# Performance work log

Hardware: AMD Instinct MI355X
Metric: run time of the kernel (lower is better)

The kernel has to match this reference:

```python
import jax, jax.numpy as jnp
import numpy as np

B, N, F, U = 4, 4096, 256, 128
NEG = -1.0e9


def setup_inputs() -> dict:
    key = jax.random.key(0)
    k1, k2, k3, k4, k5 = jax.random.split(key, 5)
    inputs = jax.random.normal(k1, (B, N, F), dtype=jnp.float32)
    # Glorot-normal-like scales
    w = jax.random.normal(k2, (F, U), dtype=jnp.float32) * np.sqrt(2.0 / (F + U)).astype(np.float32)
    ai = jax.random.normal(k3, (U, N), dtype=jnp.float32) * np.sqrt(2.0 / (U + N)).astype(np.float32)
    aj = jax.random.normal(k4, (U, N), dtype=jnp.float32) * np.sqrt(2.0 / (U + N)).astype(np.float32)
    a = (jax.random.uniform(k5, (N, N)) < 0.004).astype(jnp.float32)
    adj = jnp.maximum(a, a.T)
    return {"inputs": inputs, "w": w, "ai": ai, "aj": aj, "adj": adj}


def reference(inputs, w, ai, aj, adj):
    # f: [B, N, U]
    f = jnp.einsum('bnf,fu->bnu', inputs, w)
    # self_attn[b,i,j] = (f ai)[b,i,j]; other_attn = transpose([0,2,1]) of (f aj)
    self_attn = jnp.einsum('bnu,um->bnm', f, ai)          # [B, N, N]
    other_attn = jnp.einsum('bnu,um->bmn', f, aj)         # transposed [B, N, N]
    mask = adj + jnp.eye(N, dtype=adj.dtype)              # allow self + neighbors
    attn = self_attn + other_attn + NEG * (1.0 - mask)
    attn = jax.nn.softmax(attn, axis=1)                   # softmax over rows (axis=1)
    # out[b,j,u] = sum_i f[b,i,u] * attn[b,i,j]
    out = jnp.einsum('biu,bij->bju', f, attn)
    return jax.nn.relu(out), attn
```

## Files before the change

### kernel.cpp

```cpp
#include <hip/hip_runtime.h>
#include <hip/hip_bf16.h>

#define NN 4096
#define UU 128
#define BB 4
#define FF 256
#define MAXD 128
#define ZB 1024

typedef float fv4 __attribute__((ext_vector_type(4)));

__device__ __forceinline__ unsigned short f2bf(float x) {
    unsigned int u = __float_as_uint(x);
    unsigned int r = (u + 0x7fffu + ((u >> 16) & 1u)) >> 16;
    return (unsigned short)r;
}
__device__ __forceinline__ float bf2f(unsigned short h) {
    return __uint_as_float(((unsigned int)h) << 16);
}

template <int CTRL, int RMASK>
__device__ __forceinline__ float dpp_step(float x) {
    int ti = __builtin_amdgcn_update_dpp(0, __float_as_int(x), CTRL, RMASK, 0xf, true);
    return x + __int_as_float(ti);
}
__device__ __forceinline__ float wave_sum_dpp(float x) {
    x = dpp_step<0x111, 0xf>(x);
    x = dpp_step<0x112, 0xf>(x);
    x = dpp_step<0x114, 0xf>(x);
    x = dpp_step<0x118, 0xf>(x);
    x = dpp_step<0x142, 0xa>(x);
    x = dpp_step<0x143, 0xc>(x);
    return __int_as_float(__builtin_amdgcn_readlane(__float_as_int(x), 63));
}

__global__ __launch_bounds__(256) void transpose2(const float* __restrict__ ai,
                                                  const float* __restrict__ aj,
                                                  unsigned short* __restrict__ aiT,
                                                  unsigned short* __restrict__ ajT) {
    __shared__ float tile[32][33];
    const float* src = blockIdx.z ? aj : ai;
    unsigned short* dst = blockIdx.z ? ajT : aiT;
    int n0 = blockIdx.x * 32;
    int u0 = blockIdx.y * 32;
    int tx = threadIdx.x;
    int ty = threadIdx.y;
    for (int r = 0; r < 32; r += 8)
        tile[ty + r][tx] = src[(size_t)(u0 + ty + r) * NN + n0 + tx];
    __syncthreads();
    for (int r = 0; r < 32; r += 8)
        dst[(size_t)(n0 + ty + r) * UU + u0 + tx] = f2bf(tile[tx][ty + r]);
}

__global__ __launch_bounds__(256) void fgemm(const float* __restrict__ A,
                                             const float* __restrict__ Wm,
                                             unsigned short* __restrict__ F) {
    __shared__ float As[64][36];
    __shared__ float Ws[64][132];
    int t = threadIdx.x;
    int r0 = blockIdx.x * 32;
    int cg = t & 31;
    int rg = t >> 5;
    float acc[4][4] = {};

    for (int kc = 0; kc < FF; kc += 64) {
        {
            int row = t >> 3;
            int kb = (t & 7) * 8;
            const float* ap = A + (size_t)(r0 + row) * FF + kc + kb;
            float4 v0 = *(const float4*)(ap);
            float4 v1 = *(const float4*)(ap + 4);
            As[kb + 0][row] = v0.x; As[kb + 1][row] = v0.y;
            As[kb + 2][row] = v0.z; As[kb + 3][row] = v0.w;
            As[kb + 4][row] = v1.x; As[kb + 5][row] = v1.y;
            As[kb + 6][row] = v1.z; As[kb + 7][row] = v1.w;
        }
#pragma unroll
        for (int q = 0; q < 8; q++) {
            int idx = q * 256 + t;
            int k = idx >> 5;
            int c4 = (idx & 31) * 4;
            *(float4*)&Ws[k][c4] = *(const float4*)(Wm + (size_t)(kc + k) * UU + c4);
        }
        __syncthreads();
#pragma unroll 8
        for (int kk = 0; kk < 64; kk++) {
            float4 a4 = *(const float4*)&As[kk][rg * 4];
            float4 w4 = *(const float4*)&Ws[kk][cg * 4];
            acc[0][0] += a4.x * w4.x; acc[0][1] += a4.x * w4.y; acc[0][2] += a4.x * w4.z; acc[0][3] += a4.x * w4.w;
            acc[1][0] += a4.y * w4.x; acc[1][1] += a4.y * w4.y; acc[1][2] += a4.y * w4.z; acc[1][3] += a4.y * w4.w;
            acc[2][0] += a4.z * w4.x; acc[2][1] += a4.z * w4.y; acc[2][2] += a4.z * w4.z; acc[2][3] += a4.z * w4.w;
            acc[3][0] += a4.w * w4.x; acc[3][1] += a4.w * w4.y; acc[3][2] += a4.w * w4.z; acc[3][3] += a4.w * w4.w;
        }
        __syncthreads();
    }
#pragma unroll
    for (int i = 0; i < 4; i++) {
        ushort4 h;
        h.x = f2bf(acc[i][0]); h.y = f2bf(acc[i][1]);
        h.z = f2bf(acc[i][2]); h.w = f2bf(acc[i][3]);
        *(ushort4*)(F + (size_t)(r0 + rg * 4 + i) * UU + cg * 4) = h;
    }
}

__global__ __launch_bounds__(256) void scan_adj(const float* __restrict__ adj,
                                                unsigned short* __restrict__ csc,
                                                int* __restrict__ cnt,
                                                int* __restrict__ dblf) {
    __shared__ unsigned short tmp[MAXD];
    __shared__ int c, d;
    int j = blockIdx.x, tid = threadIdx.x;
    if (tid == 0) { c = 0; d = 0; }
    __syncthreads();
    const float4* row = (const float4*)(adj + (size_t)j * NN);
#pragma unroll
    for (int k = 0; k < 4; k++) {
        int q = tid + k * 256;
        float4 v = row[q];
        int base = q * 4;
        float vals[4] = {v.x, v.y, v.z, v.w};
#pragma unroll
        for (int t = 0; t < 4; t++) {
            int i = base + t;
            bool nz = (vals[t] != 0.0f);
            if (i == j) { if (nz) d = 1; nz = true; }
            if (nz) {
                int p = atomicAdd(&c, 1);
                if (p < MAXD) tmp[p] = (unsigned short)i;
            }
        }
    }
    __syncthreads();
    int M = c < MAXD ? c : MAXD;
    if (tid < M) csc[(size_t)j * MAXD + tid] = tmp[tid];
    if (tid == 0) { cnt[j] = M; dblf[j] = d; }
}

__global__ __launch_bounds__(256) void gat_zc(const unsigned short* __restrict__ csc,
                                              const int* __restrict__ cnt,
                                              const int* __restrict__ dblf,
                                              const unsigned short* __restrict__ f,
                                              const unsigned short* __restrict__ aiT,
                                              const unsigned short* __restrict__ ajT,
                                              float* __restrict__ out,
                                              float* __restrict__ tmpex,
                                              float* __restrict__ attn) {
    int tid = threadIdx.x;
    if (blockIdx.x >= NN) {
        size_t base = (size_t)(blockIdx.x - NN) * ((size_t)BB * NN * NN / ZB);
        fv4* p = (fv4*)(attn + base) + tid;
        fv4 z = {0.f, 0.f, 0.f, 0.f};
#pragma unroll 8
        for (int q = 0; q < 64; q++)
            __builtin_nontemporal_store(z, p + q * 256);
        return;
    }

    __shared__ unsigned short sidx[MAXD];
    int j = blockIdx.x;
    int lane = tid & 63, b = tid >> 6;
    int M = cnt[j];
    int oneh = dblf[j];
    if (tid < MAXD) sidx[tid] = csc[(size_t)j * MAXD + tid];

    const unsigned short* fb = f + (size_t)b * NN * UU;
    float* te = tmpex + ((size_t)b * NN + j) * MAXD;
    ushort2 fjh = *(const ushort2*)(fb + (size_t)j * UU + 2 * lane);
    float fjx = bf2f(fjh.x), fjy = bf2f(fjh.y);

    if (oneh) {
        int g0 = csc[(size_t)j * MAXD + lane];
        int g1 = csc[(size_t)j * MAXD + lane + 64];
        if (lane < M)      te[lane]      = (g0 == j) ? 1.0f : 0.0f;
        if (lane + 64 < M) te[lane + 64] = (g1 == j) ? 1.0f : 0.0f;
        float2 o;
        o.x = fjx > 0.0f ? fjx : 0.0f;
        o.y = fjy > 0.0f ? fjy : 0.0f;
        *(float2*)(out + ((size_t)(b * NN + j)) * UU + 2 * lane) = o;
        return;
    }
    __syncthreads();

    ushort2 aih = *(const ushort2*)(aiT + (size_t)j * UU + 2 * lane);
    float aix = bf2f(aih.x), aiy = bf2f(aih.y);
    float denom = 0.0f, acc0 = 0.0f, acc1 = 0.0f;
    float keep0 = 0.0f, keep1 = 0.0f;
    for (int e = 0; e < M; e++) {
        int i = sidx[e];
        ushort2 fih = *(const ushort2*)(fb + (size_t)i * UU + 2 * lane);
        ushort2 ajh = *(const ushort2*)(ajT + (size_t)i * UU + 2 * lane);
        float fix = bf2f(fih.x), fiy = bf2f(fih.y);
        float p = fix * aix + fiy * aiy + fjx * bf2f(ajh.x) + fjy * bf2f(ajh.y);
        float ex = __expf(wave_sum_dpp(p));
        denom += ex;
        acc0 += ex * fix;
        acc1 += ex * fiy;
        if ((e & 63) == lane) { if (e < 64) keep0 = ex; else keep1 = ex; }
    }
    float inv = 1.0f / denom;

    float2 o;
    o.x = acc0 * inv; o.y = acc1 * inv;
    o.x = o.x > 0.0f ? o.x : 0.0f;
    o.y = o.y > 0.0f ? o.y : 0.0f;
    *(float2*)(out + ((size_t)(b * NN + j)) * UU + 2 * lane) = o;

    if (lane < M)      te[lane]      = keep0 * inv;
    if (lane + 64 < M) te[lane + 64] = keep1 * inv;
}

__global__ __launch_bounds__(256) void attn_scatter(const unsigned short* __restrict__ csc,
                                                    const int* __restrict__ cnt,
                                                    const float* __restrict__ tmpex,
                                                    float* __restrict__ attn) {
    int j = blockIdx.x, tid = threadIdx.x;
    int lane = tid & 63, b = tid >> 6;
    int M = cnt[j];
    const float* te = tmpex + ((size_t)b * NN + j) * MAXD;
    if (lane < M) {
        int i = csc[(size_t)j * MAXD + lane];
        __builtin_nontemporal_store(te[lane], &attn[((size_t)(b * NN + i)) * NN + j]);
    }
    if (lane + 64 < M) {
        int i = csc[(size_t)j * MAXD + lane + 64];
        __builtin_nontemporal_store(te[lane + 64], &attn[((size_t)(b * NN + i)) * NN + j]);
    }
}

extern "C" void kernel_launch(void* const* d_in, const int* in_sizes, int n_in,
                              void* d_out, int out_size, void* d_ws, size_t ws_size,
                              hipStream_t stream) {
    const float* inputs = (const float*)d_in[0];
    const float* w      = (const float*)d_in[1];
    const float* ai     = (const float*)d_in[2];
    const float* aj     = (const float*)d_in[3];
    const float* adj    = (const float*)d_in[4];

    float* out  = (float*)d_out;
    float* attn = out + (size_t)BB * NN * UU;

    unsigned short* f   = (unsigned short*)d_ws;
    unsigned short* aiT = f + (size_t)BB * NN * UU;
    unsigned short* ajT = aiT + (size_t)NN * UU;
    unsigned short* csc = ajT + (size_t)NN * UU;
    int* cnt  = (int*)(csc + (size_t)NN * MAXD);
    int* dblf = cnt + NN;
    float* tmpex = (float*)(dblf + NN);

    transpose2<<<dim3(NN / 32, UU / 32, 2), dim3(32, 8), 0, stream>>>(ai, aj, aiT, ajT);
    fgemm<<<dim3((BB * NN) / 32), 256, 0, stream>>>(inputs, w, f);
    scan_adj<<<NN, 256, 0, stream>>>(adj, csc, cnt, dblf);
    gat_zc<<<NN + ZB, 256, 0, stream>>>(csc, cnt, dblf, f, aiT, ajT, out, tmpex, attn);
    attn_scatter<<<NN, 256, 0, stream>>>(csc, cnt, tmpex, attn);
}
```

Measured before the change: 419.2 us.

## Merge transpose, feature GEMM and adjacency scan into one launch

Combines the ai/aj transpose, the feature GEMM and the adjacency CSC scan into a single kernel that dispatches on block index, sharing one LDS buffer. This removes two kernel launches and their serialization, letting the independent stages overlap on the GPU. In exchange every block reserves the largest LDS footprint, which may lower occupancy for the scan and transpose blocks.

```diff
diff --git a/kernel.cpp b/kernel.cpp
--- a/kernel.cpp
+++ b/kernel.cpp
@@ -34,106 +34,111 @@
     return __int_as_float(__builtin_amdgcn_readlane(__float_as_int(x), 63));
 }
 
-__global__ __launch_bounds__(256) void transpose2(const float* __restrict__ ai,
-                                                  const float* __restrict__ aj,
-                                                  unsigned short* __restrict__ aiT,
-                                                  unsigned short* __restrict__ ajT) {
-    __shared__ float tile[32][33];
-    const float* src = blockIdx.z ? aj : ai;
-    unsigned short* dst = blockIdx.z ? ajT : aiT;
-    int n0 = blockIdx.x * 32;
-    int u0 = blockIdx.y * 32;
-    int tx = threadIdx.x;
-    int ty = threadIdx.y;
-    for (int r = 0; r < 32; r += 8)
-        tile[ty + r][tx] = src[(size_t)(u0 + ty + r) * NN + n0 + tx];
-    __syncthreads();
-    for (int r = 0; r < 32; r += 8)
-        dst[(size_t)(n0 + ty + r) * UU + u0 + tx] = f2bf(tile[tx][ty + r]);
-}
-
-__global__ __launch_bounds__(256) void fgemm(const float* __restrict__ A,
-                                             const float* __restrict__ Wm,
-                                             unsigned short* __restrict__ F) {
-    __shared__ float As[64][36];
-    __shared__ float Ws[64][132];
+__global__ __launch_bounds__(256) void stage1(const float* __restrict__ A,
+                                              const float* __restrict__ Wm,
+                                              const float* __restrict__ adj,
+                                              const float* __restrict__ ai,
+                                              const float* __restrict__ aj,
+                                              unsigned short* __restrict__ F,
+                                              unsigned short* __restrict__ csc,
+                                              int* __restrict__ cnt,
+                                              int* __restrict__ dblf,
+                                              unsigned short* __restrict__ aiT,
+                                              unsigned short* __restrict__ ajT) {
+    __shared__ __align__(16) char smem[43008];
     int t = threadIdx.x;
-    int r0 = blockIdx.x * 32;
-    int cg = t & 31;
-    int rg = t >> 5;
-    float acc[4][4] = {};
-
-    for (int kc = 0; kc < FF; kc += 64) {
-        {
-            int row = t >> 3;
-            int kb = (t & 7) * 8;
-            const float* ap = A + (size_t)(r0 + row) * FF + kc + kb;
-            float4 v0 = *(const float4*)(ap);
-            float4 v1 = *(const float4*)(ap + 4);
-            As[kb + 0][row] = v0.x; As[kb + 1][row] = v0.y;
-            As[kb + 2][row] = v0.z; As[kb + 3][row] = v0.w;
-            As[kb + 4][row] = v1.x; As[kb + 5][row] = v1.y;
-            As[kb + 6][row] = v1.z; As[kb + 7][row] = v1.w;
+    int bid = blockIdx.x;
+
+    if (bid < 512) {
+        float (*As)[36]  = (float(*)[36])smem;
+        float (*Ws)[132] = (float(*)[132])(smem + 9216);
+        int r0 = bid * 32;
+        int cg = t & 31;
+        int rg = t >> 5;
+        float acc[4][4] = {};
+        for (int kc = 0; kc < FF; kc += 64) {
+            {
+                int row = t >> 3;
+                int kb = (t & 7) * 8;
+                const float* ap = A + (size_t)(r0 + row) * FF + kc + kb;
+                float4 v0 = *(const float4*)(ap);
+                float4 v1 = *(const float4*)(ap + 4);
+                As[kb + 0][row] = v0.x; As[kb + 1][row] = v0.y;
+                As[kb + 2][row] = v0.z; As[kb + 3][row] = v0.w;
+                As[kb + 4][row] = v1.x; As[kb + 5][row] = v1.y;
+                As[kb + 6][row] = v1.z; As[kb + 7][row] = v1.w;
+            }
+#pragma unroll
+            for (int q = 0; q < 8; q++) {
+                int idx = q * 256 + t;
+                int k = idx >> 5;
+                int c4 = (idx & 31) * 4;
+                *(float4*)&Ws[k][c4] = *(const float4*)(Wm + (size_t)(kc + k) * UU + c4);
+            }
+            __syncthreads();
+#pragma unroll 8
+            for (int kk = 0; kk < 64; kk++) {
+                float4 a4 = *(const float4*)&As[kk][rg * 4];
+                float4 w4 = *(const float4*)&Ws[kk][cg * 4];
+                acc[0][0] += a4.x * w4.x; acc[0][1] += a4.x * w4.y; acc[0][2] += a4.x * w4.z; acc[0][3] += a4.x * w4.w;
+                acc[1][0] += a4.y * w4.x; acc[1][1] += a4.y * w4.y; acc[1][2] += a4.y * w4.z; acc[1][3] += a4.y * w4.w;
+                acc[2][0] += a4.z * w4.x; acc[2][1] += a4.z * w4.y; acc[2][2] += a4.z * w4.z; acc[2][3] += a4.z * w4.w;
+                acc[3][0] += a4.w * w4.x; acc[3][1] += a4.w * w4.y; acc[3][2] += a4.w * w4.z; acc[3][3] += a4.w * w4.w;
+            }
+            __syncthreads();
         }
 #pragma unroll
-        for (int q = 0; q < 8; q++) {
-            int idx = q * 256 + t;
-            int k = idx >> 5;
-            int c4 = (idx & 31) * 4;
-            *(float4*)&Ws[k][c4] = *(const float4*)(Wm + (size_t)(kc + k) * UU + c4);
+        for (int i = 0; i < 4; i++) {
+            ushort4 h;
+            h.x = f2bf(acc[i][0]); h.y = f2bf(acc[i][1]);
+            h.z = f2bf(acc[i][2]); h.w = f2bf(acc[i][3]);
+            *(ushort4*)(F + (size_t)(r0 + rg * 4 + i) * UU + cg * 4) = h;
+        }
+    } else if (bid < 4608) {
+        unsigned short* tmp = (unsigned short*)smem;
+        int* cd = (int*)(smem + 256);
+        int j = bid - 512;
+        if (t == 0) { cd[0] = 0; cd[1] = 0; }
+        __syncthreads();
+        const float4* row = (const float4*)(adj + (size_t)j * NN);
+#pragma unroll
+        for (int k = 0; k < 4; k++) {
+            int q = t + k * 256;
+            float4 v = row[q];
+            int base = q * 4;
+            float vals[4] = {v.x, v.y, v.z, v.w};
+#pragma unroll
+            for (int s = 0; s < 4; s++) {
+                int i = base + s;
+                bool nz = (vals[s] != 0.0f);
+                if (i == j) { if (nz) cd[1] = 1; nz = true; }
+                if (nz) {
+                    int p = atomicAdd(&cd[0], 1);
+                    if (p < MAXD) tmp[p] = (unsigned short)i;
+                }
+            }
         }
         __syncthreads();
-#pragma unroll 8
-        for (int kk = 0; kk < 64; kk++) {
-            float4 a4 = *(const float4*)&As[kk][rg * 4];
-            float4 w4 = *(const float4*)&Ws[kk][cg * 4];
-            acc[0][0] += a4.x * w4.x; acc[0][1] += a4.x * w4.y; acc[0][2] += a4.x * w4.z; acc[0][3] += a4.x * w4.w;
-            acc[1][0] += a4.y * w4.x; acc[1][1] += a4.y * w4.y; acc[1][2] += a4.y * w4.z; acc[1][3] += a4.y * w4.w;
-            acc[2][0] += a4.z * w4.x; acc[2][1] += a4.z * w4.y; acc[2][2] += a4.z * w4.z; acc[2][3] += a4.z * w4.w;
-            acc[3][0] += a4.w * w4.x; acc[3][1] += a4.w * w4.y; acc[3][2] += a4.w * w4.z; acc[3][3] += a4.w * w4.w;
-        }
+        int M = cd[0] < MAXD ? cd[0] : MAXD;
+        if (t < M) csc[(size_t)j * MAXD + t] = tmp[t];
+        if (t == 0) { cnt[j] = M; dblf[j] = cd[1]; }
+    } else {
+        float (*tile)[33] = (float(*)[33])smem;
+        int r = bid - 4608;
+        int z = r >> 9;
+        int rem = r & 511;
+        int n0 = (rem >> 2) * 32;
+        int u0 = (rem & 3) * 32;
+        const float* src = z ? aj : ai;
+        unsigned short* dst = z ? ajT : aiT;
+        int tx = t & 31;
+        int ty = t >> 5;
+        for (int rr = 0; rr < 32; rr += 8)
+            tile[ty + rr][tx] = src[(size_t)(u0 + ty + rr) * NN + n0 + tx];
         __syncthreads();
-    }
-#pragma unroll
-    for (int i = 0; i < 4; i++) {
-        ushort4 h;
-        h.x = f2bf(acc[i][0]); h.y = f2bf(acc[i][1]);
-        h.z = f2bf(acc[i][2]); h.w = f2bf(acc[i][3]);
-        *(ushort4*)(F + (size_t)(r0 + rg * 4 + i) * UU + cg * 4) = h;
-    }
-}
-
-__global__ __launch_bounds__(256) void scan_adj(const float* __restrict__ adj,
-                                                unsigned short* __restrict__ csc,
-                                                int* __restrict__ cnt,
-                                                int* __restrict__ dblf) {
-    __shared__ unsigned short tmp[MAXD];
-    __shared__ int c, d;
-    int j = blockIdx.x, tid = threadIdx.x;
-    if (tid == 0) { c = 0; d = 0; }
-    __syncthreads();
-    const float4* row = (const float4*)(adj + (size_t)j * NN);
-#pragma unroll
-    for (int k = 0; k < 4; k++) {
-        int q = tid + k * 256;
-        float4 v = row[q];
-        int base = q * 4;
-        float vals[4] = {v.x, v.y, v.z, v.w};
-#pragma unroll
-        for (int t = 0; t < 4; t++) {
-            int i = base + t;
-            bool nz = (vals[t] != 0.0f);
-            if (i == j) { if (nz) d = 1; nz = true; }
-            if (nz) {
-                int p = atomicAdd(&c, 1);
-                if (p < MAXD) tmp[p] = (unsigned short)i;
-            }
-        }
-    }
-    __syncthreads();
-    int M = c < MAXD ? c : MAXD;
-    if (tid < M) csc[(size_t)j * MAXD + tid] = tmp[tid];
-    if (tid == 0) { cnt[j] = M; dblf[j] = d; }
+        for (int rr = 0; rr < 32; rr += 8)
+            dst[(size_t)(n0 + ty + rr) * UU + u0 + tx] = f2bf(tile[tx][ty + rr]);
+    }
 }
 
 __global__ __launch_bounds__(256) void gat_zc(const unsigned short* __restrict__ csc,
@@ -247,9 +252,7 @@
     int* dblf = cnt + NN;
     float* tmpex = (float*)(dblf + NN);
 
-    transpose2<<<dim3(NN / 32, UU / 32, 2), dim3(32, 8), 0, stream>>>(ai, aj, aiT, ajT);
-    fgemm<<<dim3((BB * NN) / 32), 256, 0, stream>>>(inputs, w, f);
-    scan_adj<<<NN, 256, 0, stream>>>(adj, csc, cnt, dblf);
+    stage1<<<5632, 256, 0, stream>>>(inputs, w, adj, ai, aj, f, csc, cnt, dblf, aiT, ajT);
     gat_zc<<<NN + ZB, 256, 0, stream>>>(csc, cnt, dblf, f, aiT, ajT, out, tmpex, attn);
     attn_scatter<<<NN, 256, 0, stream>>>(csc, cnt, tmpex, attn);
 }
```

New measurement: 413.1 us. Within noise of the previous version (-1.5%).
